# Kernel tuning notes

Measured on AMD Instinct MI355X. Metric: run time of the kernel, lower is better.

The kernel has to match this reference:

```python
import jax, jax.numpy as jnp
import numpy as np

N = 100000
E = 1600000
C = 64
NOUT = 32
L = 2


def _lin(x, w, b=None):
    y = x @ w
    return y if b is None else y + b


def setup_inputs() -> dict:
    key = jax.random.key(0)
    ks = jax.random.split(key, 20)
    s = 0.1
    inp = {
        "node_feat": jax.random.normal(ks[0], (N, C), jnp.float32),
        "xyz": jax.random.normal(ks[1], (N, 3), jnp.float32),
        "src": jax.random.randint(ks[2], (E,), 0, N, jnp.int32),
        "dst": jax.random.randint(ks[3], (E,), 0, N, jnp.int32),
        # EGNN layer params, stacked over L layers
        "edge_w1": jax.random.normal(ks[4], (L, 2 * C + 1, C), jnp.float32) * s,
        "edge_b1": jnp.zeros((L, C), jnp.float32),
        "edge_w2": jax.random.normal(ks[5], (L, C, C), jnp.float32) * s,
        "edge_b2": jnp.zeros((L, C), jnp.float32),
        "coord_w1": jax.random.normal(ks[6], (L, C, C), jnp.float32) * s,
        "coord_b1": jnp.zeros((L, C), jnp.float32),
        "coord_w2": jax.random.normal(ks[7], (L, C, 1), jnp.float32) * s,  # no bias in DGL
        "node_w1": jax.random.normal(ks[8], (L, 2 * C, C), jnp.float32) * s,
        "node_b1": jnp.zeros((L, C), jnp.float32),
        "node_w2": jax.random.normal(ks[9], (L, C, C), jnp.float32) * s,
        "node_b2": jnp.zeros((L, C), jnp.float32),
        # shared LayerNorm + output head
        "ln_g": jnp.ones((C,), jnp.float32),
        "ln_b": jnp.zeros((C,), jnp.float32),
        "out_w": jax.random.normal(ks[10], (C, NOUT), jnp.float32) * s,
        "out_b": jnp.zeros((NOUT,), jnp.float32),
    }
    return inp


def _egnn_layer(h, x, src, dst, ew1, eb1, ew2, eb2, cw1, cb1, cw2, nw1, nb1, nw2, nb2):
    n = h.shape[0]
    x_diff = x[src] - x[dst]                                   # [E,3]
    radial = jnp.sum(x_diff * x_diff, axis=-1, keepdims=True)  # [E,1]
    x_diff = x_diff / (jnp.sqrt(radial) + 1e-30)
    f = jnp.concatenate([h[src], h[dst], radial], axis=-1)     # [E,2C+1]
    msg_h = jax.nn.silu(_lin(jax.nn.silu(_lin(f, ew1, eb1)), ew2, eb2))  # [E,C]
    coord_s = _lin(jax.nn.silu(_lin(msg_h, cw1, cb1)), cw2)    # [E,1]
    msg_x = coord_s * x_diff                                   # [E,3]
    h_neigh = jax.ops.segment_sum(msg_h, dst, num_segments=n)
    x_sum = jax.ops.segment_sum(msg_x, dst, num_segments=n)
    deg = jax.ops.segment_sum(jnp.ones((msg_x.shape[0], 1), msg_x.dtype), dst, num_segments=n)
    x_neigh = x_sum / jnp.maximum(deg, 1.0)                    # mean agg (0 for isolated nodes)
    x_new = x + x_neigh
    h_new = _lin(jax.nn.silu(_lin(jnp.concatenate([h, h_neigh], axis=-1), nw1, nb1)), nw2, nb2)
    return h_new, x_new


def _layernorm(x, g, b, eps=1e-5):
    mu = jnp.mean(x, axis=-1, keepdims=True)
    var = jnp.mean(jnp.square(x - mu), axis=-1, keepdims=True)
    return (x - mu) * jax.lax.rsqrt(var + eps) * g + b


def reference(node_feat, xyz, src, dst, edge_w1, edge_b1, edge_w2, edge_b2,
              coord_w1, coord_b1, coord_w2, node_w1, node_b1, node_w2, node_b2,
              ln_g, ln_b, out_w, out_b):
    h, x = node_feat, xyz
    for l in range(L):
        h, x = _egnn_layer(h, x, src, dst,
                           edge_w1[l], edge_b1[l], edge_w2[l], edge_b2[l],
                           coord_w1[l], coord_b1[l], coord_w2[l],
                           node_w1[l], node_b1[l], node_w2[l], node_b2[l])
        h = jax.nn.gelu(h, approximate=False)
        h = _layernorm(h, ln_g, ln_b)
    return _lin(h, out_w, out_b)  # [N, NOUT]
```

## Files before the change

kernel.cpp:

```cpp
#include <hip/hip_runtime.h>
#include <hip/hip_bf16.h>

#define NN 100000
#define NE 1600000
#define SW 136
#define ST 68
#define STF 68

typedef __attribute__((ext_vector_type(8))) short bf16x8;
typedef __attribute__((ext_vector_type(4))) float f32x4;

__device__ __forceinline__ unsigned short f2bf(float f) {
    union { float f; unsigned int u; } v; v.f = f;
    unsigned int u = v.u + 0x7fff + ((v.u >> 16) & 1);
    return (unsigned short)(u >> 16);
}
__device__ __forceinline__ unsigned int f2bf2u(float a, float b) {
    union { __hip_bfloat162 h; unsigned int u; } cv;
    cv.h = __float22bfloat162_rn(make_float2(a, b));
    return cv.u;
}
__device__ __forceinline__ float bf2f(unsigned short h) {
    union { unsigned int u; float f; } v; v.u = ((unsigned int)h) << 16;
    return v.f;
}
__device__ __forceinline__ float silu_f(float v) {
    return v * __builtin_amdgcn_rcpf(1.0f + __expf(-v));
}

__global__ void hist_kernel(const int* __restrict__ dst, int* __restrict__ counts) {
    int i = blockIdx.x * 256 + threadIdx.x;
    if (i < NE) atomicAdd(&counts[dst[i]], 1);
}

#define SCAN_BLK ((NN + 1023) / 1024)

__global__ __launch_bounds__(256) void scanA(const int* __restrict__ counts,
                                             int2* __restrict__ blockTot) {
    __shared__ int sS[256], sC[256];
    int tid = threadIdx.x;
    int base = blockIdx.x * 1024 + tid * 4;
    int s = 0, c = 0;
#pragma unroll
    for (int j = 0; j < 4; ++j) {
        int idx = base + j;
        if (idx < NN) { int v = counts[idx]; s += v; c += (v + 15) >> 4; }
    }
    sS[tid] = s; sC[tid] = c;
    __syncthreads();
    for (int off = 128; off > 0; off >>= 1) {
        if (tid < off) { sS[tid] += sS[tid + off]; sC[tid] += sC[tid + off]; }
        __syncthreads();
    }
    if (tid == 0) blockTot[blockIdx.x] = make_int2(sS[0], sC[0]);
}

__global__ __launch_bounds__(128) void scanB(int2* __restrict__ blockTot,
                                             int* __restrict__ rowptr,
                                             int* __restrict__ chunkPtr) {
    __shared__ int sS[128], sC[128];
    int tid = threadIdx.x;
    int2 v = (tid < SCAN_BLK) ? blockTot[tid] : make_int2(0, 0);
    sS[tid] = v.x; sC[tid] = v.y;
    __syncthreads();
    for (int off = 1; off < 128; off <<= 1) {
        int aS = sS[tid], aC = sC[tid];
        int bS = (tid >= off) ? sS[tid - off] : 0;
        int bC = (tid >= off) ? sC[tid - off] : 0;
        __syncthreads();
        sS[tid] = aS + bS; sC[tid] = aC + bC;
        __syncthreads();
    }
    if (tid < SCAN_BLK) blockTot[tid] = make_int2(sS[tid] - v.x, sC[tid] - v.y);
    if (tid == 127) { rowptr[NN] = sS[127]; chunkPtr[NN] = sC[127]; }
}

__global__ __launch_bounds__(256) void scanC(const int* __restrict__ counts,
                                             const int2* __restrict__ blockTot,
                                             int* __restrict__ rowptr,
                                             int* __restrict__ cursor,
                                             int* __restrict__ chunkPtr) {
    __shared__ int sS[256], sC[256];
    int tid = threadIdx.x;
    int base = blockIdx.x * 1024 + tid * 4;
    int vloc[4]; int s = 0, c = 0;
#pragma unroll
    for (int j = 0; j < 4; ++j) {
        int idx = base + j;
        vloc[j] = (idx < NN) ? counts[idx] : 0;
        s += vloc[j]; c += (vloc[j] + 15) >> 4;
    }
    sS[tid] = s; sC[tid] = c;
    __syncthreads();
    for (int off = 1; off < 256; off <<= 1) {
        int aS = sS[tid], aC = sC[tid];
        int bS = (tid >= off) ? sS[tid - off] : 0;
        int bC = (tid >= off) ? sC[tid - off] : 0;
        __syncthreads();
        sS[tid] = aS + bS; sC[tid] = aC + bC;
        __syncthreads();
    }
    int2 bo = blockTot[blockIdx.x];
    int runS = bo.x + sS[tid] - s;
    int runC = bo.y + sC[tid] - c;
#pragma unroll
    for (int j = 0; j < 4; ++j) {
        int idx = base + j;
        if (idx < NN) {
            rowptr[idx] = runS; cursor[idx] = runS; chunkPtr[idx] = runC;
            runS += vloc[j]; runC += (vloc[j] + 15) >> 4;
        }
    }
}

__global__ void scatter_kernel(const int* __restrict__ src, const int* __restrict__ dst,
                               int* __restrict__ cursor, int* __restrict__ srcS) {
    int i = blockIdx.x * 256 + threadIdx.x;
    if (i < NE) {
        int pos = atomicAdd(&cursor[dst[i]], 1);
        srcS[pos] = src[i];
    }
}

__global__ void fill_chunks(const int* __restrict__ rowptr, const int* __restrict__ chunkPtr,
                            int2* __restrict__ chunkTbl) {
    int n = blockIdx.x * 256 + threadIdx.x;
    if (n < NN) {
        int s = rowptr[n], e = rowptr[n + 1];
        int b = chunkPtr[n];
        for (int cs = s, i = 0; cs < e; cs += 16, ++i) {
            int len = min(16, e - cs);
            chunkTbl[b + i] = make_int2(n, cs | (len << 25));
        }
    }
}

__global__ __launch_bounds__(256, 4) void prep_kernel(
    const unsigned short* __restrict__ hbf,
    const float* __restrict__ ew1,
    const float* __restrict__ eb1,
    unsigned short* __restrict__ Ys,
    float* __restrict__ Yd)
{
    __shared__ __align__(16) unsigned short w1sT[64 * ST];
    __shared__ __align__(16) unsigned short w1dT[64 * ST];
    __shared__ float eb1s[64];

    const int tid  = threadIdx.x;
    const int wave = __builtin_amdgcn_readfirstlane(tid >> 6);
    const int lane = tid & 63;
    const int quad = lane >> 4;
    const int l15  = lane & 15;

    for (int i = tid; i < 64 * 64; i += 256) {
        int n = i & 63, k = i >> 6;
        w1sT[n * ST + k] = f2bf(ew1[k * 64 + n]);
        w1dT[n * ST + k] = f2bf(ew1[(64 + k) * 64 + n]);
    }
    if (tid < 64) eb1s[tid] = eb1[tid];
    __syncthreads();

    for (int t = blockIdx.x * 4 + wave; t < NN / 16; t += gridDim.x * 4) {
        const int n0 = t * 16;
        const unsigned short* ph = hbf + (size_t)(n0 + l15) * 64 + quad * 8;
        bf16x8 a0 = *(const bf16x8*)(ph);
        bf16x8 a1 = *(const bf16x8*)(ph + 32);

        f32x4 accS[4], accD[4];
#pragma unroll
        for (int nt = 0; nt < 4; ++nt) {
            accS[nt] = (f32x4){0.f, 0.f, 0.f, 0.f};
            accD[nt] = (f32x4){0.f, 0.f, 0.f, 0.f};
        }
        const unsigned short* bS = &w1sT[l15 * ST + quad * 8];
        const unsigned short* bD = &w1dT[l15 * ST + quad * 8];
#pragma unroll
        for (int nt = 0; nt < 4; ++nt) {
            const unsigned short* bbS = bS + nt * 16 * ST;
            const unsigned short* bbD = bD + nt * 16 * ST;
            accS[nt] = __builtin_amdgcn_mfma_f32_16x16x32_bf16(a0, *(const bf16x8*)(bbS), accS[nt], 0, 0, 0);
            accS[nt] = __builtin_amdgcn_mfma_f32_16x16x32_bf16(a1, *(const bf16x8*)(bbS + 32), accS[nt], 0, 0, 0);
            accD[nt] = __builtin_amdgcn_mfma_f32_16x16x32_bf16(a0, *(const bf16x8*)(bbD), accD[nt], 0, 0, 0);
            accD[nt] = __builtin_amdgcn_mfma_f32_16x16x32_bf16(a1, *(const bf16x8*)(bbD + 32), accD[nt], 0, 0, 0);
        }
#pragma unroll
        for (int nt = 0; nt < 4; ++nt) {
            int col = nt * 16 + l15;
#pragma unroll
            for (int r = 0; r < 4; ++r) {
                int n = n0 + quad * 4 + r;
                Ys[(size_t)n * 64 + col] = f2bf(accS[nt][r]);
                Yd[(size_t)n * 64 + col] = accD[nt][r] + eb1s[col];
            }
        }
    }
}

template <bool WRITE_X, int MINW>
__global__ __launch_bounds__(256, MINW) void edge6_kernel(
    const float4* __restrict__ x4,
    const unsigned short* __restrict__ Ys,
    const float* __restrict__ Yd,
    const int* __restrict__ srcS,
    const int2* __restrict__ chunkTbl,
    const int* __restrict__ chunkCnt,
    const float* __restrict__ ew1,
    const float* __restrict__ ew2,
    const float* __restrict__ eb2,
    const float* __restrict__ cw1,
    const float* __restrict__ cb1,
    const float* __restrict__ cw2,
    float* __restrict__ h_neigh,
    float* __restrict__ x_sum)
{
    constexpr int TWN = WRITE_X ? (4 * 16 * STF) : 4;
    __shared__ __align__(16) float tWF[TWN];
    __shared__ __align__(16) float w1ls[64];
    __shared__ float eb2s[64], cb1s[64], cw2s[64];

    const int tid  = threadIdx.x;
    const int wave = __builtin_amdgcn_readfirstlane(tid >> 6);
    const int lane = tid & 63;
    const int quad = lane >> 4;
    const int l15  = lane & 15;

    if (tid < 64) {
        eb2s[tid] = eb2[tid]; cb1s[tid] = cb1[tid];
        cw2s[tid] = cw2[tid]; w1ls[tid] = ew1[128 * 64 + tid];
    }
    bf16x8 b2[2][4], b3[2][4];
#pragma unroll
    for (int ks = 0; ks < 2; ++ks)
#pragma unroll
        for (int nt = 0; nt < 4; ++nt) {
#pragma unroll
            for (int j = 0; j < 8; ++j) {
                int k = ks * 32 + quad * 8 + j;
                ((unsigned short*)&b2[ks][nt])[j] = f2bf(ew2[k * 64 + nt * 16 + l15]);
                if (WRITE_X)
                    ((unsigned short*)&b3[ks][nt])[j] = f2bf(cw1[k * 64 + nt * 16 + l15]);
            }
        }
    __syncthreads();

    float* tW = tWF + wave * 16 * STF;
    const int C  = chunkCnt[0];
    const int gw = blockIdx.x * 4 + wave;
    const int nw = gridDim.x * 4;

    float4 wl0 = *(const float4*)&w1ls[quad * 8];
    float4 wl1 = *(const float4*)&w1ls[quad * 8 + 4];
    float4 wl2 = *(const float4*)&w1ls[32 + quad * 8];
    float4 wl3 = *(const float4*)&w1ls[32 + quad * 8 + 4];

    for (int idx = gw; idx < C; idx += nw) {
        const int2 ck = chunkTbl[idx];
        const int n   = __builtin_amdgcn_readfirstlane(ck.x);
        const int cky = __builtin_amdgcn_readfirstlane(ck.y);
        const int cs  = cky & 0x01FFFFFF;
        const int len = ((unsigned)cky) >> 25;

        const int s = srcS[cs + ((l15 < len) ? l15 : 0)];
        const float4 xn = x4[n];
        const float4 xs = x4[s];
        const float dx = xs.x - xn.x;
        const float dy = xs.y - xn.y;
        const float dz = xs.z - xn.z;
        const float radL = dx * dx + dy * dy + dz * dz;
        float xdx = 0.f, xdy = 0.f, xdz = 0.f;
        if (WRITE_X) {
            float inv = __builtin_amdgcn_rcpf(__builtin_amdgcn_sqrtf(radL) + 1e-30f);
            xdx = dx * inv; xdy = dy * inv; xdz = dz * inv;
        }

        float cxR[4], cyR[4], czR[4]; bool valR[4];
#pragma unroll
        for (int r = 0; r < 4; ++r) {
            int er = quad * 4 + r;
            valR[r] = er < len;
            if (WRITE_X) {
                cxR[r] = __shfl(xdx, er);
                cyR[r] = __shfl(xdy, er);
                czR[r] = __shfl(xdz, er);
            }
        }

        const unsigned short* ps = Ys + (size_t)s * 64 + quad * 8;
        bf16x8 g0 = *(const bf16x8*)(ps);
        bf16x8 g1 = *(const bf16x8*)(ps + 32);
        const float* pyd = Yd + (size_t)n * 64 + quad * 8;
        float4 y0 = *(const float4*)(pyd);
        float4 y1 = *(const float4*)(pyd + 4);
        float4 y2 = *(const float4*)(pyd + 32);
        float4 y3 = *(const float4*)(pyd + 36);

        bf16x8 aF0, aF1;
        {
            const unsigned short* pg0 = (const unsigned short*)&g0;
            const unsigned short* pg1 = (const unsigned short*)&g1;
            float t0[8], t1v[8];
            const float* py0 = (const float*)&y0;
            const float* py1 = (const float*)&y1;
            const float* pw0 = (const float*)&wl0;
            const float* pw1 = (const float*)&wl1;
            const float* py2 = (const float*)&y2;
            const float* py3 = (const float*)&y3;
            const float* pw2 = (const float*)&wl2;
            const float* pw3 = (const float*)&wl3;
#pragma unroll
            for (int j = 0; j < 4; ++j) {
                t0[j]      = silu_f(bf2f(pg0[j])     + py0[j] + radL * pw0[j]);
                t0[j + 4]  = silu_f(bf2f(pg0[j + 4]) + py1[j] + radL * pw1[j]);
                t1v[j]     = silu_f(bf2f(pg1[j])     + py2[j] + radL * pw2[j]);
                t1v[j + 4] = silu_f(bf2f(pg1[j + 4]) + py3[j] + radL * pw3[j]);
            }
            unsigned int* pa0 = (unsigned int*)&aF0;
            unsigned int* pa1 = (unsigned int*)&aF1;
#pragma unroll
            for (int j = 0; j < 4; ++j) {
                pa0[j] = f2bf2u(t0[j * 2], t0[j * 2 + 1]);
                pa1[j] = f2bf2u(t1v[j * 2], t1v[j * 2 + 1]);
            }
        }

        f32x4 acc2[4];
#pragma unroll
        for (int nt = 0; nt < 4; ++nt) acc2[nt] = (f32x4){0.f, 0.f, 0.f, 0.f};
#pragma unroll
        for (int nt = 0; nt < 4; ++nt) {
            acc2[nt] = __builtin_amdgcn_mfma_f32_16x16x32_bf16(aF0, b2[0][nt], acc2[nt], 0, 0, 0);
            acc2[nt] = __builtin_amdgcn_mfma_f32_16x16x32_bf16(aF1, b2[1][nt], acc2[nt], 0, 0, 0);
        }
#pragma unroll
        for (int nt = 0; nt < 4; ++nt) {
            int col = nt * 16 + l15;
            float colsum = 0.f;
#pragma unroll
            for (int r = 0; r < 4; ++r) {
                float v = silu_f(acc2[nt][r] + eb2s[col]);
                if (valR[r]) colsum += v;
                if (WRITE_X) tW[(quad * 4 + r) * STF + col] = v;
            }
            colsum += __shfl_xor(colsum, 16);
            colsum += __shfl_xor(colsum, 32);
            if (quad == 0) atomicAdd(&h_neigh[(size_t)n * 64 + col], colsum);
        }
        if (WRITE_X) {
            bf16x8 aG0, aG1;
            {
                const float* pf = &tW[l15 * STF + quad * 8];
                float4 u0 = *(const float4*)(pf);
                float4 u1 = *(const float4*)(pf + 4);
                float4 u2 = *(const float4*)(pf + 32);
                float4 u3 = *(const float4*)(pf + 36);
                unsigned int* pa0 = (unsigned int*)&aG0;
                unsigned int* pa1 = (unsigned int*)&aG1;
                pa0[0] = f2bf2u(u0.x, u0.y); pa0[1] = f2bf2u(u0.z, u0.w);
                pa0[2] = f2bf2u(u1.x, u1.y); pa0[3] = f2bf2u(u1.z, u1.w);
                pa1[0] = f2bf2u(u2.x, u2.y); pa1[1] = f2bf2u(u2.z, u2.w);
                pa1[2] = f2bf2u(u3.x, u3.y); pa1[3] = f2bf2u(u3.z, u3.w);
            }
            f32x4 acc3[4];
#pragma unroll
            for (int nt = 0; nt < 4; ++nt) acc3[nt] = (f32x4){0.f, 0.f, 0.f, 0.f};
#pragma unroll
            for (int nt = 0; nt < 4; ++nt) {
                acc3[nt] = __builtin_amdgcn_mfma_f32_16x16x32_bf16(aG0, b3[0][nt], acc3[nt], 0, 0, 0);
                acc3[nt] = __builtin_amdgcn_mfma_f32_16x16x32_bf16(aG1, b3[1][nt], acc3[nt], 0, 0, 0);
            }
            float part_[4] = {0.f, 0.f, 0.f, 0.f};
#pragma unroll
            for (int nt = 0; nt < 4; ++nt) {
                int col = nt * 16 + l15;
#pragma unroll
                for (int r = 0; r < 4; ++r)
                    part_[r] += silu_f(acc3[nt][r] + cb1s[col]) * cw2s[col];
            }
            float xc = 0.f;
#pragma unroll
            for (int r = 0; r < 4; ++r) {
                float p = part_[r];
                p += __shfl_xor(p, 1);
                p += __shfl_xor(p, 2);
                p += __shfl_xor(p, 4);
                p += __shfl_xor(p, 8);
                if (valR[r]) {
                    float comp = (l15 == 0) ? cxR[r] : (l15 == 1) ? cyR[r] : czR[r];
                    xc += p * comp;
                }
            }
            xc += __shfl_xor(xc, 16);
            xc += __shfl_xor(xc, 32);
            if (quad == 0 && l15 < 3)
                atomicAdd(&x_sum[(size_t)n * 3 + l15], xc);
        }
    }
}

__global__ void xupd(const float* __restrict__ x_sum, const int* __restrict__ rowptr,
                     const float4* __restrict__ xin, float4* __restrict__ xout) {
    int n = blockIdx.x * 256 + threadIdx.x;
    if (n < NN) {
        float d = (float)(rowptr[n + 1] - rowptr[n]);
        float id = __builtin_amdgcn_rcpf(fmaxf(d, 1.0f));
        float4 v = xin[n];
        v.x += x_sum[n * 3 + 0] * id;
        v.y += x_sum[n * 3 + 1] * id;
        v.z += x_sum[n * 3 + 2] * id;
        v.w = 0.f;
        xout[n] = v;
    }
}

template <bool DO_HEAD>
__global__ __launch_bounds__(256, 4) void node_kernel(
    unsigned short* hbf,
    const float* __restrict__ h_nb,
    const float* __restrict__ nw1,
    const float* __restrict__ nb1,
    const float* __restrict__ nw2,
    const float* __restrict__ nb2,
    const float* __restrict__ ln_g,
    const float* __restrict__ ln_b,
    const float* __restrict__ out_w,
    const float* __restrict__ out_b,
    float* __restrict__ out)
{
    __shared__ __align__(16) unsigned short w1T[64 * SW];
    __shared__ __align__(16) unsigned short w2T[64 * ST];
    __shared__ __align__(16) unsigned short tAll[4 * 16 * ST];
    __shared__ float nb1s[64], nb2s[64], gs[64], bs[64], obs[32];

    const int tid  = threadIdx.x;
    const int wave = __builtin_amdgcn_readfirstlane(tid >> 6);
    const int lane = tid & 63;
    const int quad = lane >> 4;
    const int l15  = lane & 15;

    for (int i = tid; i < 64 * 128; i += 256) {
        int n = i & 63, k = i >> 6;
        w1T[n * SW + k] = f2bf(nw1[k * 64 + n]);
    }
    for (int i = tid; i < 64 * 64; i += 256) {
        int n = i & 63, k = i >> 6;
        w2T[n * ST + k] = f2bf(nw2[k * 64 + n]);
    }
    if (tid < 64) {
        nb1s[tid] = nb1[tid]; nb2s[tid] = nb2[tid];
        gs[tid] = ln_g[tid]; bs[tid] = ln_b[tid];
        if (DO_HEAD && tid < 32) obs[tid] = out_b[tid];
    }
    bf16x8 b3[2][2];
    if (DO_HEAD) {
#pragma unroll
        for (int ks = 0; ks < 2; ++ks)
#pragma unroll
            for (int nt = 0; nt < 2; ++nt) {
#pragma unroll
                for (int j = 0; j < 8; ++j) {
                    int k = ks * 32 + quad * 8 + j;
                    ((unsigned short*)&b3[ks][nt])[j] = f2bf(out_w[k * 32 + nt * 16 + l15]);
                }
            }
    }
    __syncthreads();

    unsigned short* tW = tAll + wave * 16 * ST;

    for (int t = blockIdx.x * 4 + wave; t < NN / 16; t += gridDim.x * 4) {
        const int n0 = t * 16;
        const int myRow = n0 + l15;
        const unsigned short* ph = hbf + (size_t)myRow * 64 + quad * 8;
        bf16x8 a0 = *(const bf16x8*)(ph);
        bf16x8 a1 = *(const bf16x8*)(ph + 32);
        bf16x8 a2, a3;
        {
            const float* pb = h_nb + (size_t)myRow * 64 + quad * 8;
            float4 v0 = *(const float4*)(pb);
            float4 v1 = *(const float4*)(pb + 4);
            float4 v2 = *(const float4*)(pb + 32);
            float4 v3 = *(const float4*)(pb + 36);
            unsigned int* pa2 = (unsigned int*)&a2;
            unsigned int* pa3 = (unsigned int*)&a3;
            pa2[0] = f2bf2u(v0.x, v0.y); pa2[1] = f2bf2u(v0.z, v0.w);
            pa2[2] = f2bf2u(v1.x, v1.y); pa2[3] = f2bf2u(v1.z, v1.w);
            pa3[0] = f2bf2u(v2.x, v2.y); pa3[1] = f2bf2u(v2.z, v2.w);
            pa3[2] = f2bf2u(v3.x, v3.y); pa3[3] = f2bf2u(v3.z, v3.w);
        }

        f32x4 acc[4];
#pragma unroll
        for (int nt = 0; nt < 4; ++nt) acc[nt] = (f32x4){0.f, 0.f, 0.f, 0.f};
        {
            const unsigned short* bBase = &w1T[l15 * SW + quad * 8];
#pragma unroll
            for (int nt = 0; nt < 4; ++nt) {
                const unsigned short* bb = bBase + nt * 16 * SW;
                acc[nt] = __builtin_amdgcn_mfma_f32_16x16x32_bf16(a0, *(const bf16x8*)(bb), acc[nt], 0, 0, 0);
                acc[nt] = __builtin_amdgcn_mfma_f32_16x16x32_bf16(a1, *(const bf16x8*)(bb + 32), acc[nt], 0, 0, 0);
                acc[nt] = __builtin_amdgcn_mfma_f32_16x16x32_bf16(a2, *(const bf16x8*)(bb + 64), acc[nt], 0, 0, 0);
                acc[nt] = __builtin_amdgcn_mfma_f32_16x16x32_bf16(a3, *(const bf16x8*)(bb + 96), acc[nt], 0, 0, 0);
            }
        }
#pragma unroll
        for (int nt = 0; nt < 4; ++nt) {
            int col = nt * 16 + l15;
#pragma unroll
            for (int r = 0; r < 4; ++r) {
                float v = acc[nt][r] + nb1s[col];
                tW[(quad * 4 + r) * ST + col] = f2bf(silu_f(v));
            }
        }
        f32x4 acc2[4];
#pragma unroll
        for (int nt = 0; nt < 4; ++nt) acc2[nt] = (f32x4){0.f, 0.f, 0.f, 0.f};
        {
            bf16x8 ax0 = *(const bf16x8*)&tW[l15 * ST + quad * 8];
            bf16x8 ax1 = *(const bf16x8*)&tW[l15 * ST + 32 + quad * 8];
            const unsigned short* bBase = &w2T[l15 * ST + quad * 8];
#pragma unroll
            for (int nt = 0; nt < 4; ++nt) {
                const unsigned short* bb = bBase + nt * 16 * ST;
                acc2[nt] = __builtin_amdgcn_mfma_f32_16x16x32_bf16(ax0, *(const bf16x8*)(bb), acc2[nt], 0, 0, 0);
                acc2[nt] = __builtin_amdgcn_mfma_f32_16x16x32_bf16(ax1, *(const bf16x8*)(bb + 32), acc2[nt], 0, 0, 0);
            }
        }
        float vals[4][4];
        float sum[4] = {0.f, 0.f, 0.f, 0.f}, ss[4] = {0.f, 0.f, 0.f, 0.f};
#pragma unroll
        for (int nt = 0; nt < 4; ++nt) {
            int col = nt * 16 + l15;
#pragma unroll
            for (int r = 0; r < 4; ++r) {
                float v = acc2[nt][r] + nb2s[col];
                float g = 0.5f * v * (1.0f + erff(v * 0.70710678118654752f));
                vals[nt][r] = g;
                sum[r] += g;
                ss[r] += g * g;
            }
        }
#pragma unroll
        for (int r = 0; r < 4; ++r) {
            float s1 = sum[r], s2 = ss[r];
            s1 += __shfl_xor(s1, 1); s2 += __shfl_xor(s2, 1);
            s1 += __shfl_xor(s1, 2); s2 += __shfl_xor(s2, 2);
            s1 += __shfl_xor(s1, 4); s2 += __shfl_xor(s2, 4);
            s1 += __shfl_xor(s1, 8); s2 += __shfl_xor(s2, 8);
            sum[r] = s1; ss[r] = s2;
        }
#pragma unroll
        for (int r = 0; r < 4; ++r) {
            float mean = sum[r] * (1.0f / 64.0f);
            float var  = ss[r] * (1.0f / 64.0f) - mean * mean;
            float rstd = rsqrtf(var + 1e-5f);
            int n = n0 + quad * 4 + r;
#pragma unroll
            for (int nt = 0; nt < 4; ++nt) {
                int col = nt * 16 + l15;
                float y = (vals[nt][r] - mean) * rstd * gs[col] + bs[col];
                if (DO_HEAD) tW[(quad * 4 + r) * ST + col] = f2bf(y);
                else hbf[(size_t)n * 64 + col] = f2bf(y);
            }
        }
        if (DO_HEAD) {
            f32x4 accH[2];
#pragma unroll
            for (int nt = 0; nt < 2; ++nt) accH[nt] = (f32x4){0.f, 0.f, 0.f, 0.f};
            bf16x8 ax0 = *(const bf16x8*)&tW[l15 * ST + quad * 8];
            bf16x8 ax1 = *(const bf16x8*)&tW[l15 * ST + 32 + quad * 8];
#pragma unroll
            for (int nt = 0; nt < 2; ++nt) {
                accH[nt] = __builtin_amdgcn_mfma_f32_16x16x32_bf16(ax0, b3[0][nt], accH[nt], 0, 0, 0);
                accH[nt] = __builtin_amdgcn_mfma_f32_16x16x32_bf16(ax1, b3[1][nt], accH[nt], 0, 0, 0);
            }
#pragma unroll
            for (int nt = 0; nt < 2; ++nt) {
                int col = nt * 16 + l15;
#pragma unroll
                for (int r = 0; r < 4; ++r)
                    out[(size_t)(n0 + quad * 4 + r) * 32 + col] = accH[nt][r] + obs[col];
            }
        }
    }
}

__global__ void init_h(const float* __restrict__ nf, unsigned short* __restrict__ hbf) {
    int i = blockIdx.x * 256 + threadIdx.x;
    if (i < NN * 64) hbf[i] = f2bf(nf[i]);
}
__global__ void init_x(const float* __restrict__ xyz, float4* __restrict__ x4) {
    int n = blockIdx.x * 256 + threadIdx.x;
    if (n < NN) {
        float4 v;
        v.x = xyz[n * 3 + 0]; v.y = xyz[n * 3 + 1]; v.z = xyz[n * 3 + 2]; v.w = 0.f;
        x4[n] = v;
    }
}

extern "C" void kernel_launch(void* const* d_in, const int* in_sizes, int n_in,
                              void* d_out, int out_size, void* d_ws, size_t ws_size,
                              hipStream_t stream)
{
    const float* node_feat = (const float*)d_in[0];
    const float* xyz   = (const float*)d_in[1];
    const int*   src   = (const int*)d_in[2];
    const int*   dst   = (const int*)d_in[3];
    const float* ew1   = (const float*)d_in[4];
    const float* eb1   = (const float*)d_in[5];
    const float* ew2   = (const float*)d_in[6];
    const float* eb2   = (const float*)d_in[7];
    const float* cw1   = (const float*)d_in[8];
    const float* cb1   = (const float*)d_in[9];
    const float* cw2   = (const float*)d_in[10];
    const float* nw1   = (const float*)d_in[11];
    const float* nb1   = (const float*)d_in[12];
    const float* nw2   = (const float*)d_in[13];
    const float* nb2   = (const float*)d_in[14];
    const float* ln_g  = (const float*)d_in[15];
    const float* ln_b  = (const float*)d_in[16];
    const float* out_w = (const float*)d_in[17];
    const float* out_b = (const float*)d_in[18];
    float* out = (float*)d_out;

    char* ws = (char*)d_ws;
    float* h_neigh = (float*)ws;                 ws += (size_t)NN * 64 * 4;
    unsigned short* hbf = (unsigned short*)ws;   ws += (size_t)NN * 64 * 2;
    unsigned short* Ys  = (unsigned short*)ws;   ws += (size_t)NN * 64 * 2;
    float* Yd     = (float*)ws;                  ws += (size_t)NN * 64 * 4;
    float4* xA    = (float4*)ws;                 ws += (size_t)NN * 16;
    float4* xB    = (float4*)ws;                 ws += (size_t)NN * 16;
    float* x_sum  = (float*)ws;                  ws += (size_t)NN * 3 * 4;
    int* rowptr   = (int*)ws;                    ws += (size_t)(NN + 1) * 4;
    int* chunkPtr = (int*)ws;                    ws += (size_t)(NN + 1) * 4;
    int* counts   = (int*)ws;                    ws += (size_t)NN * 4;
    int* srcS     = (int*)ws;                    ws += (size_t)NE * 4;
    int2* chunkTbl = (int2*)ws;                  ws += (size_t)(NN + NE / 16) * 8;
    int2* blockTot = (int2*)ws;                  ws += (size_t)SCAN_BLK * 8;

    hipMemsetAsync(counts, 0, (size_t)NN * 4, stream);
    init_h<<<(NN * 64 + 255) / 256, 256, 0, stream>>>(node_feat, hbf);
    init_x<<<(NN + 255) / 256, 256, 0, stream>>>(xyz, xA);
    hist_kernel<<<(NE + 255) / 256, 256, 0, stream>>>(dst, counts);
    scanA<<<SCAN_BLK, 256, 0, stream>>>(counts, blockTot);
    scanB<<<1, 128, 0, stream>>>(blockTot, rowptr, chunkPtr);
    scanC<<<SCAN_BLK, 256, 0, stream>>>(counts, blockTot, rowptr, counts, chunkPtr);
    scatter_kernel<<<(NE + 255) / 256, 256, 0, stream>>>(src, dst, counts, srcS);
    fill_chunks<<<(NN + 255) / 256, 256, 0, stream>>>(rowptr, chunkPtr, chunkTbl);

    hipMemsetAsync(h_neigh, 0, (size_t)NN * 64 * 4, stream);
    hipMemsetAsync(x_sum, 0, (size_t)NN * 3 * 4, stream);
    prep_kernel<<<1024, 256, 0, stream>>>(hbf, ew1, eb1, Ys, Yd);
    edge6_kernel<true, 3><<<2048, 256, 0, stream>>>(
        xA, Ys, Yd, srcS, chunkTbl, chunkPtr + NN,
        ew1, ew2, eb2, cw1, cb1, cw2, h_neigh, x_sum);
    xupd<<<(NN + 255) / 256, 256, 0, stream>>>(x_sum, rowptr, xA, xB);
    node_kernel<false><<<1024, 256, 0, stream>>>(
        hbf, h_neigh, nw1, nb1, nw2, nb2, ln_g, ln_b, out_w, out_b, out);

    hipMemsetAsync(h_neigh, 0, (size_t)NN * 64 * 4, stream);
    prep_kernel<<<1024, 256, 0, stream>>>(hbf, ew1 + 129 * 64, eb1 + 64, Ys, Yd);
    edge6_kernel<false, 4><<<2048, 256, 0, stream>>>(
        xB, Ys, Yd, srcS, chunkTbl, chunkPtr + NN,
        ew1 + 129 * 64, ew2 + 64 * 64, eb2 + 64, cw1 + 64 * 64, cb1 + 64, cw2 + 64,
        h_neigh, nullptr);
    node_kernel<true><<<1024, 256, 0, stream>>>(
        hbf, h_neigh, nw1 + 128 * 64, nb1 + 64, nw2 + 64 * 64, nb2 + 64,
        ln_g, ln_b, out_w, out_b, out);
}
```

Before: 781.4 us.

## Move edge MLP weights to LDS, store staging in bf16, fuse init_h with prep

The edge kernel now keeps the second edge-layer and coord-layer weight fragments in shared memory as transposed bf16 tiles instead of holding them in registers. This frees VGPRs so launch bounds can rise to 5 waves-per-SIMD for both layers. The per-wave staging tile is now stored as bf16 rather than fp32, which removes the reload-and-convert step before the coord MFMA and halves its LDS footprint. Separately, the bf16 conversion of node features is fused into the first-layer prep GEMM kernel, dropping one launch and one pass over hbf. The cost is extra LDS reads on every MFMA B operand and more LDS per block.

After: 980.6 us. 1.25x slower.

```diff
diff --git a/kernel.cpp b/kernel.cpp
--- a/kernel.cpp
+++ b/kernel.cpp
@@ -5,7 +5,6 @@
 #define NE 1600000
 #define SW 136
 #define ST 68
-#define STF 68
 
 typedef __attribute__((ext_vector_type(8))) short bf16x8;
 typedef __attribute__((ext_vector_type(4))) float f32x4;
@@ -135,6 +134,82 @@
     }
 }
 
+__global__ __launch_bounds__(256, 4) void initprep_kernel(
+    const float* __restrict__ nf,
+    const float* __restrict__ ew1,
+    const float* __restrict__ eb1,
+    unsigned short* __restrict__ hbf,
+    unsigned short* __restrict__ Ys,
+    float* __restrict__ Yd)
+{
+    __shared__ __align__(16) unsigned short w1sT[64 * ST];
+    __shared__ __align__(16) unsigned short w1dT[64 * ST];
+    __shared__ float eb1s[64];
+
+    const int tid  = threadIdx.x;
+    const int wave = __builtin_amdgcn_readfirstlane(tid >> 6);
+    const int lane = tid & 63;
+    const int quad = lane >> 4;
+    const int l15  = lane & 15;
+
+    for (int i = tid; i < 64 * 64; i += 256) {
+        int n = i & 63, k = i >> 6;
+        w1sT[n * ST + k] = f2bf(ew1[k * 64 + n]);
+        w1dT[n * ST + k] = f2bf(ew1[(64 + k) * 64 + n]);
+    }
+    if (tid < 64) eb1s[tid] = eb1[tid];
+    __syncthreads();
+
+    for (int t = blockIdx.x * 4 + wave; t < NN / 16; t += gridDim.x * 4) {
+        const int n0 = t * 16;
+        const int myRow = n0 + l15;
+        const float* pf = nf + (size_t)myRow * 64 + quad * 8;
+        float4 v0 = *(const float4*)(pf);
+        float4 v1 = *(const float4*)(pf + 4);
+        float4 v2 = *(const float4*)(pf + 32);
+        float4 v3 = *(const float4*)(pf + 36);
+        bf16x8 a0, a1;
+        {
+            unsigned int* pa0 = (unsigned int*)&a0;
+            unsigned int* pa1 = (unsigned int*)&a1;
+            pa0[0] = f2bf2u(v0.x, v0.y); pa0[1] = f2bf2u(v0.z, v0.w);
+            pa0[2] = f2bf2u(v1.x, v1.y); pa0[3] = f2bf2u(v1.z, v1.w);
+            pa1[0] = f2bf2u(v2.x, v2.y); pa1[1] = f2bf2u(v2.z, v2.w);
+            pa1[2] = f2bf2u(v3.x, v3.y); pa1[3] = f2bf2u(v3.z, v3.w);
+        }
+        *(bf16x8*)(hbf + (size_t)myRow * 64 + quad * 8) = a0;
+        *(bf16x8*)(hbf + (size_t)myRow * 64 + 32 + quad * 8) = a1;
+
+        f32x4 accS[4], accD[4];
+#pragma unroll
+        for (int nt = 0; nt < 4; ++nt) {
+            accS[nt] = (f32x4){0.f, 0.f, 0.f, 0.f};
+            accD[nt] = (f32x4){0.f, 0.f, 0.f, 0.f};
+        }
+        const unsigned short* bS = &w1sT[l15 * ST + quad * 8];
+        const unsigned short* bD = &w1dT[l15 * ST + quad * 8];
+#pragma unroll
+        for (int nt = 0; nt < 4; ++nt) {
+            const unsigned short* bbS = bS + nt * 16 * ST;
+            const unsigned short* bbD = bD + nt * 16 * ST;
+            accS[nt] = __builtin_amdgcn_mfma_f32_16x16x32_bf16(a0, *(const bf16x8*)(bbS), accS[nt], 0, 0, 0);
+            accS[nt] = __builtin_amdgcn_mfma_f32_16x16x32_bf16(a1, *(const bf16x8*)(bbS + 32), accS[nt], 0, 0, 0);
+            accD[nt] = __builtin_amdgcn_mfma_f32_16x16x32_bf16(a0, *(const bf16x8*)(bbD), accD[nt], 0, 0, 0);
+            accD[nt] = __builtin_amdgcn_mfma_f32_16x16x32_bf16(a1, *(const bf16x8*)(bbD + 32), accD[nt], 0, 0, 0);
+        }
+#pragma unroll
+        for (int nt = 0; nt < 4; ++nt) {
+            int col = nt * 16 + l15;
+#pragma unroll
+            for (int r = 0; r < 4; ++r) {
+                int n = n0 + quad * 4 + r;
+                Ys[(size_t)n * 64 + col] = f2bf(accS[nt][r]);
+                Yd[(size_t)n * 64 + col] = accD[nt][r] + eb1s[col];
+            }
+        }
+    }
+}
+
 __global__ __launch_bounds__(256, 4) void prep_kernel(
     const unsigned short* __restrict__ hbf,
     const float* __restrict__ ew1,
@@ -196,8 +271,8 @@
     }
 }
 
-template <bool WRITE_X, int MINW>
-__global__ __launch_bounds__(256, MINW) void edge6_kernel(
+template <bool WRITE_X>
+__global__ __launch_bounds__(256, 5) void edge7_kernel(
     const float4* __restrict__ x4,
     const unsigned short* __restrict__ Ys,
     const float* __restrict__ Yd,
@@ -213,8 +288,11 @@
     float* __restrict__ h_neigh,
     float* __restrict__ x_sum)
 {
-    constexpr int TWN = WRITE_X ? (4 * 16 * STF) : 4;
-    __shared__ __align__(16) float tWF[TWN];
+    __shared__ __align__(16) unsigned short w2T[64 * ST];
+    constexpr int C1N = WRITE_X ? (64 * ST) : 8;
+    __shared__ __align__(16) unsigned short c1T[C1N];
+    constexpr int TWN = WRITE_X ? (4 * 16 * ST) : 8;
+    __shared__ __align__(16) unsigned short tAll[TWN];
     __shared__ __align__(16) float w1ls[64];
     __shared__ float eb2s[64], cb1s[64], cw2s[64];
 
@@ -224,26 +302,18 @@
     const int quad = lane >> 4;
     const int l15  = lane & 15;
 
+    for (int i = tid; i < 64 * 64; i += 256) {
+        int n = i & 63, k = i >> 6;
+        w2T[n * ST + k] = f2bf(ew2[k * 64 + n]);
+        if (WRITE_X) c1T[n * ST + k] = f2bf(cw1[k * 64 + n]);
+    }
     if (tid < 64) {
         eb2s[tid] = eb2[tid]; cb1s[tid] = cb1[tid];
         cw2s[tid] = cw2[tid]; w1ls[tid] = ew1[128 * 64 + tid];
     }
-    bf16x8 b2[2][4], b3[2][4];
-#pragma unroll
-    for (int ks = 0; ks < 2; ++ks)
-#pragma unroll
-        for (int nt = 0; nt < 4; ++nt) {
-#pragma unroll
-            for (int j = 0; j < 8; ++j) {
-                int k = ks * 32 + quad * 8 + j;
-                ((unsigned short*)&b2[ks][nt])[j] = f2bf(ew2[k * 64 + nt * 16 + l15]);
-                if (WRITE_X)
-                    ((unsigned short*)&b3[ks][nt])[j] = f2bf(cw1[k * 64 + nt * 16 + l15]);
-            }
-        }
     __syncthreads();
 
-    float* tW = tWF + wave * 16 * STF;
+    unsigned short* tW = tAll + (WRITE_X ? wave * 16 * ST : 0);
     const int C  = chunkCnt[0];
     const int gw = blockIdx.x * 4 + wave;
     const int nw = gridDim.x * 4;
@@ -326,10 +396,14 @@
         f32x4 acc2[4];
 #pragma unroll
         for (int nt = 0; nt < 4; ++nt) acc2[nt] = (f32x4){0.f, 0.f, 0.f, 0.f};
-#pragma unroll
-        for (int nt = 0; nt < 4; ++nt) {
-            acc2[nt] = __builtin_amdgcn_mfma_f32_16x16x32_bf16(aF0, b2[0][nt], acc2[nt], 0, 0, 0);
-            acc2[nt] = __builtin_amdgcn_mfma_f32_16x16x32_bf16(aF1, b2[1][nt], acc2[nt], 0, 0, 0);
+        {
+            const unsigned short* bB = &w2T[l15 * ST + quad * 8];
+#pragma unroll
+            for (int nt = 0; nt < 4; ++nt) {
+                const unsigned short* bb = bB + nt * 16 * ST;
+                acc2[nt] = __builtin_amdgcn_mfma_f32_16x16x32_bf16(aF0, *(const bf16x8*)(bb), acc2[nt], 0, 0, 0);
+                acc2[nt] = __builtin_amdgcn_mfma_f32_16x16x32_bf16(aF1, *(const bf16x8*)(bb + 32), acc2[nt], 0, 0, 0);
+            }
         }
 #pragma unroll
         for (int nt = 0; nt < 4; ++nt) {
@@ -339,34 +413,26 @@
             for (int r = 0; r < 4; ++r) {
                 float v = silu_f(acc2[nt][r] + eb2s[col]);
                 if (valR[r]) colsum += v;
-                if (WRITE_X) tW[(quad * 4 + r) * STF + col] = v;
+                if (WRITE_X) tW[(quad * 4 + r) * ST + col] = f2bf(v);
             }
             colsum += __shfl_xor(colsum, 16);
             colsum += __shfl_xor(colsum, 32);
             if (quad == 0) atomicAdd(&h_neigh[(size_t)n * 64 + col], colsum);
         }
         if (WRITE_X) {
-            bf16x8 aG0, aG1;
+            bf16x8 aG0 = *(const bf16x8*)&tW[l15 * ST + quad * 8];
+            bf16x8 aG1 = *(const bf16x8*)&tW[l15 * ST + 32 + quad * 8];
+            f32x4 acc3[4];
+#pragma unroll
+            for (int nt = 0; nt < 4; ++nt) acc3[nt] = (f32x4){0.f, 0.f, 0.f, 0.f};
             {
-                const float* pf = &tW[l15 * STF + quad * 8];
-                float4 u0 = *(const float4*)(pf);
-                float4 u1 = *(const float4*)(pf + 4);
-                float4 u2 = *(const float4*)(pf + 32);
-                float4 u3 = *(const float4*)(pf + 36);
-                unsigned int* pa0 = (unsigned int*)&aG0;
-                unsigned int* pa1 = (unsigned int*)&aG1;
-                pa0[0] = f2bf2u(u0.x, u0.y); pa0[1] = f2bf2u(u0.z, u0.w);
-                pa0[2] = f2bf2u(u1.x, u1.y); pa0[3] = f2bf2u(u1.z, u1.w);
-                pa1[0] = f2bf2u(u2.x, u2.y); pa1[1] = f2bf2u(u2.z, u2.w);
-                pa1[2] = f2bf2u(u3.x, u3.y); pa1[3] = f2bf2u(u3.z, u3.w);
-            }
-            f32x4 acc3[4];
-#pragma unroll
-            for (int nt = 0; nt < 4; ++nt) acc3[nt] = (f32x4){0.f, 0.f, 0.f, 0.f};
-#pragma unroll
-            for (int nt = 0; nt < 4; ++nt) {
-                acc3[nt] = __builtin_amdgcn_mfma_f32_16x16x32_bf16(aG0, b3[0][nt], acc3[nt], 0, 0, 0);
-                acc3[nt] = __builtin_amdgcn_mfma_f32_16x16x32_bf16(aG1, b3[1][nt], acc3[nt], 0, 0, 0);
+                const unsigned short* bB = &c1T[l15 * ST + quad * 8];
+#pragma unroll
+                for (int nt = 0; nt < 4; ++nt) {
+                    const unsigned short* bb = bB + nt * 16 * ST;
+                    acc3[nt] = __builtin_amdgcn_mfma_f32_16x16x32_bf16(aG0, *(const bf16x8*)(bb), acc3[nt], 0, 0, 0);
+                    acc3[nt] = __builtin_amdgcn_mfma_f32_16x16x32_bf16(aG1, *(const bf16x8*)(bb + 32), acc3[nt], 0, 0, 0);
+                }
             }
             float part_[4] = {0.f, 0.f, 0.f, 0.f};
 #pragma unroll
@@ -584,10 +650,6 @@
     }
 }
 
-__global__ void init_h(const float* __restrict__ nf, unsigned short* __restrict__ hbf) {
-    int i = blockIdx.x * 256 + threadIdx.x;
-    if (i < NN * 64) hbf[i] = f2bf(nf[i]);
-}
 __global__ void init_x(const float* __restrict__ xyz, float4* __restrict__ x4) {
     int n = blockIdx.x * 256 + threadIdx.x;
     if (n < NN) {
@@ -638,8 +700,8 @@
     int2* blockTot = (int2*)ws;                  ws += (size_t)SCAN_BLK * 8;
 
     hipMemsetAsync(counts, 0, (size_t)NN * 4, stream);
-    init_h<<<(NN * 64 + 255) / 256, 256, 0, stream>>>(node_feat, hbf);
     init_x<<<(NN + 255) / 256, 256, 0, stream>>>(xyz, xA);
+    initprep_kernel<<<1024, 256, 0, stream>>>(node_feat, ew1, eb1, hbf, Ys, Yd);
     hist_kernel<<<(NE + 255) / 256, 256, 0, stream>>>(dst, counts);
     scanA<<<SCAN_BLK, 256, 0, stream>>>(counts, blockTot);
     scanB<<<1, 128, 0, stream>>>(blockTot, rowptr, chunkPtr);
@@ -649,8 +711,7 @@
 
     hipMemsetAsync(h_neigh, 0, (size_t)NN * 64 * 4, stream);
     hipMemsetAsync(x_sum, 0, (size_t)NN * 3 * 4, stream);
-    prep_kernel<<<1024, 256, 0, stream>>>(hbf, ew1, eb1, Ys, Yd);
-    edge6_kernel<true, 3><<<2048, 256, 0, stream>>>(
+    edge7_kernel<true><<<2048, 256, 0, stream>>>(
         xA, Ys, Yd, srcS, chunkTbl, chunkPtr + NN,
         ew1, ew2, eb2, cw1, cb1, cw2, h_neigh, x_sum);
     xupd<<<(NN + 255) / 256, 256, 0, stream>>>(x_sum, rowptr, xA, xB);
@@ -659,7 +720,7 @@
 
     hipMemsetAsync(h_neigh, 0, (size_t)NN * 64 * 4, stream);
     prep_kernel<<<1024, 256, 0, stream>>>(hbf, ew1 + 129 * 64, eb1 + 64, Ys, Yd);
-    edge6_kernel<false, 4><<<2048, 256, 0, stream>>>(
+    edge7_kernel<false><<<2048, 256, 0, stream>>>(
         xB, Ys, Yd, srcS, chunkTbl, chunkPtr + NN,
         ew1 + 129 * 64, ew2 + 64 * 64, eb2 + 64, cw1 + 64 * 64, cb1 + 64, cw2 + 64,
         h_neigh, nullptr);
```
